# Performance work log

Hardware: AMD Instinct MI355X
Metric: run time of the kernel (lower is better)

Reference implementation:

```python
import jax, jax.numpy as jnp
import numpy as np

EBIT = 8
BITS = 8  # wl_activate


def block_quantize_global(data, bits):
    """SWALP block quantize, scalar/global path (small_block='None', dim<=4).

    max-abs reduce -> floor(log2) exponent, clamped to signed ebit range ->
    scale -> round-to-nearest-even -> clamp to signed `bits` range -> rescale.
    If max-abs is exactly 0, data is returned unchanged.
    """
    max_entry = jnp.max(jnp.abs(data))
    # guard log2(0); result unused when max_entry == 0
    safe_max = jnp.where(max_entry == 0, jnp.float32(1.0), max_entry)
    max_exponent = jnp.floor(jnp.log2(safe_max))
    emin = -(2.0 ** (EBIT - 1))
    emax = 2.0 ** (EBIT - 1) - 1
    max_exponent = jnp.clip(max_exponent, emin, emax)
    scale = jnp.exp2(-max_exponent + (bits - 2))
    i = jnp.round(data * scale)  # torch.round_ and jnp.round both round half-to-even
    qmin = -(2.0 ** (bits - 1))
    qmax = 2.0 ** (bits - 1) - 1
    i = jnp.clip(i, qmin, qmax)
    out = i * jnp.exp2(max_exponent - (bits - 2))
    return jnp.where(max_entry == 0, data, out)


def setup_inputs() -> dict:
    key = jax.random.key(0)
    x = jax.random.normal(key, (64, 256, 56, 56), dtype=jnp.float32)
    return {"x": x}


def reference(x):
    return block_quantize_global(x, BITS)
```

## Files before the change

kernel.cpp:

```cpp
#include <hip/hip_runtime.h>
#include <math.h>


#define NB0 256
#define NT 256
#define SAMPLE_N 200704
#define NB 7168
#define CH 7
#define GRID1 2048

typedef float v4f __attribute__((ext_vector_type(4)));

__device__ inline int exp_floor(float m) {
    int eb = (int)((__float_as_uint(m) >> 23) & 0xff);
    int e = (eb == 0) ? -120 : eb - 127;
    return max(-120, min(127, e));
}
__device__ inline float exp2i(int k) {
    return __uint_as_float((unsigned)(k + 127) << 23);
}
__device__ inline float absmax4(v4f v) {
    return fmaxf(fmaxf(fabsf(v.x), fabsf(v.y)), fmaxf(fabsf(v.z), fabsf(v.w)));
}
__device__ inline v4f quant4(v4f v, float s, float inv) {
    float a = fminf(fmaxf(rintf(v.x * s), -128.0f), 127.0f);
    float b = fminf(fmaxf(rintf(v.y * s), -128.0f), 127.0f);
    float c = fminf(fmaxf(rintf(v.z * s), -128.0f), 127.0f);
    float d = fminf(fmaxf(rintf(v.w * s), -128.0f), 127.0f);
    v4f r;
    r.x = a * inv; r.y = b * inv; r.z = c * inv; r.w = d * inv;
    return r;
}
__device__ inline float block_max_reduce(float m, int t) {
    #pragma unroll
    for (int off = 32; off > 0; off >>= 1)
        m = fmaxf(m, __shfl_xor(m, off, 64));
    __shared__ float sm[4];
    if ((t & 63) == 0) sm[t >> 6] = m;
    __syncthreads();
    return fmaxf(fmaxf(sm[0], sm[1]), fmaxf(sm[2], sm[3]));
}

__global__ __launch_bounds__(NT) void bq_sample(const float* __restrict__ x,
                                                float* __restrict__ ws2) {
    const v4f* __restrict__ x4 = (const v4f*)x;
    const int gtid = blockIdx.x * NT + threadIdx.x;
    float m = 0.0f;
    for (int i = gtid; i < SAMPLE_N; i += NB0 * NT)
        m = fmaxf(m, absmax4(x4[(size_t)i << 6]));
    const float mb = block_max_reduce(m, threadIdx.x);
    if (threadIdx.x == 0) ws2[blockIdx.x] = mb;
}

__global__ __launch_bounds__(NT) void bq_spec(const float* __restrict__ x,
                                              float* __restrict__ out,
                                              float* __restrict__ partial,
                                              const float* __restrict__ ws2) {
    const v4f* __restrict__ x4 = (const v4f*)x + (size_t)blockIdx.x * (NT * CH);
    v4f* __restrict__ o4 = (v4f*)out + (size_t)blockIdx.x * (NT * CH);
    const int t = threadIdx.x;

    v4f v[CH];
    #pragma unroll
    for (int k = 0; k < CH; ++k)
        v[k] = x4[k * NT + t];

    float m = ws2[t];
    #pragma unroll
    for (int k = 0; k < CH; ++k)
        m = fmaxf(m, absmax4(v[k]));
    const float mb = block_max_reduce(m, t);
    if (t == 0) partial[blockIdx.x] = mb;

    const int e = exp_floor(mb);
    const float s = exp2i(6 - e), inv = exp2i(e - 6);
    #pragma unroll
    for (int k = 0; k < CH; ++k)
        __builtin_nontemporal_store(quant4(v[k], s, inv), &o4[k * NT + t]);
}

__global__ __launch_bounds__(NT) void bq_fix(const float* __restrict__ x,
                                             float* __restrict__ out,
                                             const float* __restrict__ partial) {
    const int t = threadIdx.x;
    float g = 0.0f;
    #pragma unroll
    for (int k = 0; k < NB / NT; ++k)
        g = fmaxf(g, partial[t + k * NT]);
    const float mg = block_max_reduce(g, t);
    const int eg = exp_floor(mg);

    if (exp_floor(partial[blockIdx.x]) == eg) return;

    const v4f* __restrict__ x4 = (const v4f*)x + (size_t)blockIdx.x * (NT * CH);
    v4f* __restrict__ o4 = (v4f*)out + (size_t)blockIdx.x * (NT * CH);
    const float s = exp2i(6 - eg), inv = exp2i(eg - 6);
    #pragma unroll
    for (int k = 0; k < CH; ++k)
        __builtin_nontemporal_store(quant4(x4[k * NT + t], s, inv), &o4[k * NT + t]);
}


__global__ __launch_bounds__(256) void bq_absmax(const float* __restrict__ x,
                                                 float* __restrict__ partial,
                                                 int n) {
    const int n4 = n >> 2;
    const v4f* __restrict__ x4 = (const v4f*)x;
    int tid = blockIdx.x * blockDim.x + threadIdx.x;
    int stride = gridDim.x * blockDim.x;
    float m = 0.0f;
    for (int i = tid; i < n4; i += stride) m = fmaxf(m, absmax4(x4[i]));
    for (int i = (n4 << 2) + tid; i < n; i += stride) m = fmaxf(m, fabsf(x[i]));
    const float mb = block_max_reduce(m, threadIdx.x);
    if (threadIdx.x == 0) partial[blockIdx.x] = mb;
}

__global__ __launch_bounds__(256) void bq_quant(const float* __restrict__ x,
                                                float* __restrict__ out,
                                                const float* __restrict__ partial,
                                                int n) {
    float bm = 0.0f;
    #pragma unroll
    for (int k = 0; k < GRID1 / 256; ++k)
        bm = fmaxf(bm, partial[threadIdx.x + k * 256]);
    const float maxe = block_max_reduce(bm, threadIdx.x);

    const int n4 = n >> 2;
    const v4f* __restrict__ x4 = (const v4f*)x;
    v4f* __restrict__ o4 = (v4f*)out;
    const int tid = blockIdx.x * blockDim.x + threadIdx.x;
    const int T = gridDim.x * blockDim.x;

    if (maxe == 0.0f) {
        for (int i = tid; i < n4; i += T)
            __builtin_nontemporal_store(x4[i], &o4[i]);
        for (int i = (n4 << 2) + tid; i < n; i += T) out[i] = x[i];
        return;
    }
    int e = ilogbf(maxe);
    e = max(-128, min(127, e));
    const float scale    = ldexpf(1.0f, -e + 6);
    const float invscale = ldexpf(1.0f, e - 6);
    for (int i = tid; i < n4; i += T)
        __builtin_nontemporal_store(quant4(x4[i], scale, invscale), &o4[i]);
    for (int i = (n4 << 2) + tid; i < n; i += T) {
        float a = rintf(x[i] * scale);
        a = fminf(fmaxf(a, -128.0f), 127.0f);
        out[i] = a * invscale;
    }
}

extern "C" void kernel_launch(void* const* d_in, const int* in_sizes, int n_in,
                              void* d_out, int out_size, void* d_ws, size_t ws_size,
                              hipStream_t stream) {
    const float* x = (const float*)d_in[0];
    float* out = (float*)d_out;
    int n = in_sizes[0];

    float* partial = (float*)d_ws;
    float* ws2 = partial + NB;
    const size_t need = (size_t)(NB + NB0) * sizeof(float);

    const long need_n = (long)NB * NT * CH * 4;
    if ((long)n == need_n && ws_size >= need) {
        hipLaunchKernelGGL(bq_sample, dim3(NB0), dim3(NT), 0, stream, x, ws2);
        hipLaunchKernelGGL(bq_spec,   dim3(NB),  dim3(NT), 0, stream, x, out, partial, ws2);
        hipLaunchKernelGGL(bq_fix,    dim3(NB),  dim3(NT), 0, stream, x, out, partial);
    } else {
        hipLaunchKernelGGL(bq_absmax, dim3(GRID1), dim3(256), 0, stream, x, partial, n);
        hipLaunchKernelGGL(bq_quant,  dim3(GRID1), dim3(256), 0, stream, x, out, partial, n);
    }
}
```

Before: 77.35 us.

## Quantize with sampled global exponent and fix up whole tensor on mismatch

The sampling kernel now reads one strided vector per thread, and the main kernel quantizes every element in a single grid-stride streaming pass. That pass uses the exponent of the sampled global max rather than a per-block one, and records true per-block maxima at the same time. A single-block check kernel compares the exponents and sets a flag, and a fixall kernel requantizes the entire tensor only when the flag is set. This drops the register-held chunk and per-block fix logic in favour of a flat streaming pass, at the risk of a full extra pass if the sample misses the true max exponent. The main loop iterates chunks in reverse order, apparently to improve cache reuse with the sample kernel.

```diff
diff --git a/kernel.cpp b/kernel.cpp
--- a/kernel.cpp
+++ b/kernel.cpp
@@ -2,11 +2,12 @@
 #include <math.h>
 
 
+#define NT 256
 #define NB0 256
-#define NT 256
-#define SAMPLE_N 200704
-#define NB 7168
-#define CH 7
+#define SAMPLE_STRIDE 196
+#define NB1 2048
+#define MG_SLOT 260
+#define FLAG_SLOT 261
 #define GRID1 2048
 
 typedef float v4f __attribute__((ext_vector_type(4)));
@@ -32,10 +33,11 @@
     return r;
 }
 __device__ inline float block_max_reduce(float m, int t) {
+    __shared__ float sm[4];
+    __syncthreads();
     #pragma unroll
     for (int off = 32; off > 0; off >>= 1)
         m = fmaxf(m, __shfl_xor(m, off, 64));
-    __shared__ float sm[4];
     if ((t & 63) == 0) sm[t >> 6] = m;
     __syncthreads();
     return fmaxf(fmaxf(sm[0], sm[1]), fmaxf(sm[2], sm[3]));
@@ -45,59 +47,73 @@
                                                 float* __restrict__ ws2) {
     const v4f* __restrict__ x4 = (const v4f*)x;
     const int gtid = blockIdx.x * NT + threadIdx.x;
-    float m = 0.0f;
-    for (int i = gtid; i < SAMPLE_N; i += NB0 * NT)
-        m = fmaxf(m, absmax4(x4[(size_t)i << 6]));
+    float m = absmax4(x4[(size_t)gtid * SAMPLE_STRIDE]);
     const float mb = block_max_reduce(m, threadIdx.x);
     if (threadIdx.x == 0) ws2[blockIdx.x] = mb;
 }
 
-__global__ __launch_bounds__(NT) void bq_spec(const float* __restrict__ x,
+__global__ __launch_bounds__(NT) void bq_main(const float* __restrict__ x,
                                               float* __restrict__ out,
                                               float* __restrict__ partial,
-                                              const float* __restrict__ ws2) {
-    const v4f* __restrict__ x4 = (const v4f*)x + (size_t)blockIdx.x * (NT * CH);
-    v4f* __restrict__ o4 = (v4f*)out + (size_t)blockIdx.x * (NT * CH);
-    const int t = threadIdx.x;
+                                              const float* __restrict__ ws2,
+                                              int n4) {
+    const int t = threadIdx.x, lane = t & 63;
+    float msv = fmaxf(fmaxf(ws2[lane], ws2[lane + 64]),
+                      fmaxf(ws2[lane + 128], ws2[lane + 192]));
+    #pragma unroll
+    for (int off = 32; off > 0; off >>= 1)
+        msv = fmaxf(msv, __shfl_xor(msv, off, 64));
+    const int es = exp_floor(msv);
+    const float s = exp2i(6 - es), inv = exp2i(es - 6);
 
-    v4f v[CH];
-    #pragma unroll
-    for (int k = 0; k < CH; ++k)
-        v[k] = x4[k * NT + t];
+    const v4f* __restrict__ x4 = (const v4f*)x;
+    v4f* __restrict__ o4 = (v4f*)out;
+    const int tid = blockIdx.x * NT + t;
+    const int T = NB1 * NT;
+    const int C = (n4 + T - 1) / T;
 
-    float m = ws2[t];
-    #pragma unroll
-    for (int k = 0; k < CH; ++k)
-        m = fmaxf(m, absmax4(v[k]));
+    float m = 0.0f;
+    for (int c = C - 1; c >= 0; --c) {
+        int i = c * T + tid;
+        if (i < n4) {
+            v4f v = x4[i];
+            m = fmaxf(m, absmax4(v));
+            __builtin_nontemporal_store(quant4(v, s, inv), &o4[i]);
+        }
+    }
     const float mb = block_max_reduce(m, t);
     if (t == 0) partial[blockIdx.x] = mb;
-
-    const int e = exp_floor(mb);
-    const float s = exp2i(6 - e), inv = exp2i(e - 6);
-    #pragma unroll
-    for (int k = 0; k < CH; ++k)
-        __builtin_nontemporal_store(quant4(v[k], s, inv), &o4[k * NT + t]);
 }
 
-__global__ __launch_bounds__(NT) void bq_fix(const float* __restrict__ x,
-                                             float* __restrict__ out,
-                                             const float* __restrict__ partial) {
+__global__ __launch_bounds__(NT) void bq_check(const float* __restrict__ partial,
+                                               float* __restrict__ ws2) {
     const int t = threadIdx.x;
     float g = 0.0f;
     #pragma unroll
-    for (int k = 0; k < NB / NT; ++k)
+    for (int k = 0; k < NB1 / NT; ++k)
         g = fmaxf(g, partial[t + k * NT]);
     const float mg = block_max_reduce(g, t);
+    const float ms = block_max_reduce(ws2[t], t);
+    if (t == 0) {
+        ws2[MG_SLOT] = mg;
+        ws2[FLAG_SLOT] = (exp_floor(ms) != exp_floor(mg)) ? 1.0f : 0.0f;
+    }
+}
+
+__global__ __launch_bounds__(NT) void bq_fixall(const float* __restrict__ x,
+                                                float* __restrict__ out,
+                                                const float* __restrict__ ws2,
+                                                int n4) {
+    if (ws2[FLAG_SLOT] == 0.0f) return;
+    const float mg = ws2[MG_SLOT];
+    if (mg == 0.0f) return;
     const int eg = exp_floor(mg);
-
-    if (exp_floor(partial[blockIdx.x]) == eg) return;
-
-    const v4f* __restrict__ x4 = (const v4f*)x + (size_t)blockIdx.x * (NT * CH);
-    v4f* __restrict__ o4 = (v4f*)out + (size_t)blockIdx.x * (NT * CH);
     const float s = exp2i(6 - eg), inv = exp2i(eg - 6);
-    #pragma unroll
-    for (int k = 0; k < CH; ++k)
-        __builtin_nontemporal_store(quant4(x4[k * NT + t], s, inv), &o4[k * NT + t]);
+    const v4f* __restrict__ x4 = (const v4f*)x;
+    v4f* __restrict__ o4 = (v4f*)out;
+    const int tid = blockIdx.x * NT + threadIdx.x;
+    for (int i = tid; i < n4; i += NB1 * NT)
+        __builtin_nontemporal_store(quant4(x4[i], s, inv), &o4[i]);
 }
 
 
@@ -156,16 +172,17 @@
     const float* x = (const float*)d_in[0];
     float* out = (float*)d_out;
     int n = in_sizes[0];
+    const int n4 = n >> 2;
 
     float* partial = (float*)d_ws;
-    float* ws2 = partial + NB;
-    const size_t need = (size_t)(NB + NB0) * sizeof(float);
+    float* ws2 = partial + NB1;
+    const size_t need = (size_t)(NB1 + 264) * sizeof(float);
 
-    const long need_n = (long)NB * NT * CH * 4;
-    if ((long)n == need_n && ws_size >= need) {
+    if ((n & 3) == 0 && n4 >= NB0 * NT * SAMPLE_STRIDE && ws_size >= need) {
         hipLaunchKernelGGL(bq_sample, dim3(NB0), dim3(NT), 0, stream, x, ws2);
-        hipLaunchKernelGGL(bq_spec,   dim3(NB),  dim3(NT), 0, stream, x, out, partial, ws2);
-        hipLaunchKernelGGL(bq_fix,    dim3(NB),  dim3(NT), 0, stream, x, out, partial);
+        hipLaunchKernelGGL(bq_main,   dim3(NB1), dim3(NT), 0, stream, x, out, partial, ws2, n4);
+        hipLaunchKernelGGL(bq_check,  dim3(1),   dim3(NT), 0, stream, partial, ws2);
+        hipLaunchKernelGGL(bq_fixall, dim3(NB1), dim3(NT), 0, stream, x, out, ws2, n4);
     } else {
         hipLaunchKernelGGL(bq_absmax, dim3(GRID1), dim3(256), 0, stream, x, partial, n);
         hipLaunchKernelGGL(bq_quant,  dim3(GRID1), dim3(256), 0, stream, x, out, partial, n);
```

New measurement: 76.34 us. About the same (-1.3%).
